# Optimization experiments

Measured on AMD Instinct MI355X. Metric: run time of the kernel, lower is better.

## Reference

```python
import jax, jax.numpy as jnp
import numpy as np

B, H, D = 128, 64, 64  # batch, num_heads, head_dim; einsum structure forces seq n == m == D and H == D


def setup_inputs() -> dict:
    rng = jax.random.key(0)
    ks = jax.random.split(rng, 6)
    query = jax.random.normal(ks[0], (B, H, D, D), jnp.float32)
    key = jax.random.normal(ks[1], (B, H, D, D), jnp.float32) * 0.02
    value = jax.random.normal(ks[2], (B, H, D, D), jnp.float32) * 0.02
    memory_key = jax.random.normal(ks[3], (H, D, D), jnp.float32) * 0.02
    memory_norm = jax.random.uniform(ks[4], (H,), jnp.float32)
    memory_value = jax.random.normal(ks[5], (H, D, D), jnp.float32) * 0.02
    compression_rate = jnp.ones((H,), jnp.float32)
    return {"query": query, "key": key, "value": value,
            "memory_key": memory_key, "memory_norm": memory_norm,
            "memory_value": memory_value, "compression_rate": compression_rate}


def reference(query, key, value, memory_key, memory_norm, memory_value, compression_rate):
    h = memory_norm.shape[0]
    d = memory_key.shape[-1]

    # ---- update(key, value): associative binding + running stats (torch no_grad block) ----
    # binding in fp16 then cast to fp32, exactly as the source einsum does
    binding = jnp.einsum('bhnd,bhmd->bhnm',
                         key.astype(jnp.float16),
                         value.astype(jnp.float16)).astype(jnp.float32)
    mean_binding = binding.reshape(-1, h).mean(axis=0)            # [H] (row-major flatten, as torch .view)
    k_flat = key.reshape(-1, h, d)                                # [B*N, H, D]
    v_flat = value.reshape(-1, h, d)
    mean_value = v_flat.mean(axis=0)                              # [H, D]
    mean_key_norm = jnp.linalg.norm(k_flat.mean(axis=0), axis=-1) # [H]
    # source resets memory_key to zeros [H, D] (shape check always fires), then addcmul_
    new_memory_key = mean_binding[:, None] * mean_value           # [H, D]
    new_memory_norm = memory_norm + mean_key_norm                 # [H]
    # conditional adaptive compression
    factor = jnp.where(new_memory_norm.mean() > 0.9, compression_rate,
                       jnp.ones_like(compression_rate))
    new_memory_key = jax.lax.stop_gradient(new_memory_key * factor[:, None])
    new_memory_norm = jax.lax.stop_gradient(new_memory_norm * factor)

    # ---- retrieve(query): normalized linear-attention readout ----
    scores = jnp.einsum('bhnd,hnm->bhmd',
                        query.astype(jnp.float16),
                        memory_key.astype(jnp.float16)).astype(jnp.float32)
    # source broadcasts memory_norm [H] over the trailing dim (valid since H == D)
    scores = scores / (memory_norm + 1e-6)
    memory_output = jnp.einsum('bhmd,hnm->bhnd', scores, memory_value)
    return memory_output, scores, new_memory_key, new_memory_norm
```

## Files before the change

### kernel.cpp

```cpp
#include <hip/hip_runtime.h>
#include <hip/hip_fp16.h>

typedef _Float16 f16x8 __attribute__((ext_vector_type(8)));
typedef float f32x4 __attribute__((ext_vector_type(4)));

__device__ __forceinline__ f32x4 ntld4(const float* p) {
    return __builtin_nontemporal_load((const f32x4*)p);
}
__device__ __forceinline__ f32x4 ld4(const float* p) {
    return *(const f32x4*)p;
}
__device__ __forceinline__ void ntst4(float* p, f32x4 v) {
    __builtin_nontemporal_store(v, (f32x4*)p);
}

__global__ __launch_bounds__(256) void prep(
    const float* __restrict__ mk, const float* __restrict__ mv,
    _Float16* __restrict__ mkTb, _Float16* __restrict__ Wb)
{
    __shared__ _Float16 mks[64][72];
    __shared__ _Float16 mvs[64][72];
    const int t = threadIdx.x;
    const int h = blockIdx.x;
    const float* mkb = mk + h * 4096;
    const float* mvb = mv + h * 4096;
    {
        const int nn = t >> 2, m0 = (t & 3) * 16;
        f32x4 a0 = ld4(mkb + nn * 64 + m0),     a1 = ld4(mkb + nn * 64 + m0 + 4);
        f32x4 a2 = ld4(mkb + nn * 64 + m0 + 8), a3 = ld4(mkb + nn * 64 + m0 + 12);
        f32x4 b0 = ld4(mvb + nn * 64 + m0),     b1 = ld4(mvb + nn * 64 + m0 + 4);
        f32x4 b2 = ld4(mvb + nn * 64 + m0 + 8), b3 = ld4(mvb + nn * 64 + m0 + 12);
        f16x8 k0, k1, v0, v1;
#pragma unroll
        for (int i = 0; i < 4; ++i) {
            k0[i] = (_Float16)a0[i]; k0[i + 4] = (_Float16)a1[i];
            k1[i] = (_Float16)a2[i]; k1[i + 4] = (_Float16)a3[i];
            v0[i] = (_Float16)b0[i]; v0[i + 4] = (_Float16)b1[i];
            v1[i] = (_Float16)b2[i]; v1[i + 4] = (_Float16)b3[i];
        }
        *(f16x8*)&mks[nn][m0]     = k0;
        *(f16x8*)&mks[nn][m0 + 8] = k1;
        *(f16x8*)&mvs[nn][m0]     = v0;
        *(f16x8*)&mvs[nn][m0 + 8] = v1;
    }
    __syncthreads();
    const int w = t >> 6, l = t & 63, lr = l & 15, lk = l >> 4;
    f32x4 acc[4] = {};
#pragma unroll
    for (int kn = 0; kn < 2; ++kn) {
        f16x8 bfr = *(const f16x8*)&mks[16 * w + lr][kn * 32 + lk * 8];
#pragma unroll
        for (int di = 0; di < 4; ++di) {
            f16x8 afr = *(const f16x8*)&mvs[16 * di + lr][kn * 32 + lk * 8];
            acc[di] = __builtin_amdgcn_mfma_f32_16x16x32_f16(afr, bfr, acc[di], 0, 0, 0);
        }
    }
#pragma unroll
    for (int di = 0; di < 4; ++di)
#pragma unroll
        for (int r = 0; r < 4; ++r)
            Wb[h * 4096 + (16 * di + 4 * lk + r) * 64 + 16 * w + lr] = (_Float16)acc[di][r];
    {
        const int m = t & 63, n0 = (t >> 6) * 16;
        f16x8 x0, x1;
#pragma unroll
        for (int i = 0; i < 8; ++i) { x0[i] = mks[n0 + i][m]; x1[i] = mks[n0 + 8 + i][m]; }
        *(f16x8*)&mkTb[h * 4096 + m * 64 + n0]     = x0;
        *(f16x8*)&mkTb[h * 4096 + m * 64 + n0 + 8] = x1;
    }
}

__global__ __launch_bounds__(256) void mega(
    const float* __restrict__ q,   const float* __restrict__ key,
    const float* __restrict__ val, const _Float16* __restrict__ mkTb,
    const float* __restrict__ mnorm, const _Float16* __restrict__ Wb,
    float* __restrict__ out_mo, float* __restrict__ out_sc,
    float* __restrict__ skp, float* __restrict__ svp, float* __restrict__ pbp,
    const int nbR)
{
    __shared__ struct { float ktile[64][68]; float red[256]; float ks[64]; } smr;

    const int t   = threadIdx.x;
    const int bid = blockIdx.x;

    if (bid < nbR) {
        const int r0 = t >> 4;
        const int c0 = (t & 15) << 2;
        f32x4 ska[4] = {}; f32x4 sva[4] = {};
        float pba[4] = {0.f, 0.f, 0.f, 0.f};
        f32x4 ka[4], va[4];
        int i = bid;
#pragma unroll
        for (int qq = 0; qq < 4; ++qq) {
            const int row = r0 + 16 * qq;
            ka[qq] = ntld4(key + (size_t)i * 4096 + row * 64 + c0);
            va[qq] = ntld4(val + (size_t)i * 4096 + row * 64 + c0);
        }
        while (true) {
            const int inx = i + nbR;
            const bool more = (inx < 8192);
            f32x4 kn4[4], vn4[4];
            if (more) {
#pragma unroll
                for (int qq = 0; qq < 4; ++qq) {
                    const int row = r0 + 16 * qq;
                    kn4[qq] = ntld4(key + (size_t)inx * 4096 + row * 64 + c0);
                    vn4[qq] = ntld4(val + (size_t)inx * 4096 + row * 64 + c0);
                }
            }
#pragma unroll
            for (int qq = 0; qq < 4; ++qq) {
                const int row = r0 + 16 * qq;
                ska[qq] += ka[qq];
                sva[qq] += va[qq];
                *(f32x4*)&smr.ktile[row][c0] = ka[qq];
            }
            __syncthreads();
            {
                const int d  = t & 63;
                const int rr = (t >> 6) * 16;
                float p = 0.f;
#pragma unroll
                for (int r = 0; r < 16; ++r) p += smr.ktile[rr + r][d];
                smr.red[t] = p;
            }
            __syncthreads();
            if (t < 64)
                smr.ks[t] = smr.red[t] + smr.red[t + 64] + smr.red[t + 128] + smr.red[t + 192];
            __syncthreads();
#pragma unroll
            for (int qq = 0; qq < 4; ++qq) {
                float pq = va[qq][0] * smr.ks[c0]     + va[qq][1] * smr.ks[c0 + 1]
                         + va[qq][2] * smr.ks[c0 + 2] + va[qq][3] * smr.ks[c0 + 3];
                pq += __shfl_xor(pq, 1);
                pq += __shfl_xor(pq, 2);
                pq += __shfl_xor(pq, 4);
                pq += __shfl_xor(pq, 8);
                pba[qq] += pq;
            }
            if (!more) break;
#pragma unroll
            for (int qq = 0; qq < 4; ++qq) { ka[qq] = kn4[qq]; va[qq] = vn4[qq]; }
            i = inx;
        }
        const size_t pb4 = (size_t)bid * 4096;
#pragma unroll
        for (int qq = 0; qq < 4; ++qq) {
            ntst4(skp + pb4 + 4 * t + 1024 * qq, ska[qq]);
            ntst4(svp + pb4 + 4 * t + 1024 * qq, sva[qq]);
        }
        if ((t & 15) == 0) {
#pragma unroll
            for (int qq = 0; qq < 4; ++qq)
                pbp[bid * 64 + r0 + 16 * qq] = pba[qq];
        }
        return;
    }

    const int fid = bid - nbR;
    const int h   = fid >> 7;
    const int b   = fid & 127;
    const int bh  = b * 64 + h;
    const float* qb = q + (size_t)bh * 4096;

    const int w  = t >> 6;
    const int l  = t & 63;
    const int lr = l & 15;
    const int lk = l >> 4;

    f16x8 bfrK[2], bfrW[2];
    {
        const _Float16* mrow = mkTb + h * 4096 + (16 * w + lr) * 64 + lk * 8;
        const _Float16* wrow = Wb   + h * 4096 + (16 * w + lr) * 64 + lk * 8;
        bfrK[0] = *(const f16x8*)(mrow);
        bfrK[1] = *(const f16x8*)(mrow + 32);
        bfrW[0] = *(const f16x8*)(wrow);
        bfrW[1] = *(const f16x8*)(wrow + 32);
    }
    f32x4 scl[4];
#pragma unroll
    for (int di = 0; di < 4; ++di) {
        f32x4 nv = ld4(mnorm + 16 * di + 4 * lk);
#pragma unroll
        for (int r = 0; r < 4; ++r) scl[di][r] = __builtin_amdgcn_rcpf(nv[r] + 1e-6f);
    }

    f16x8 afr[4][2];
#pragma unroll
    for (int di = 0; di < 4; ++di) {
        const float* qcol = qb + 16 * di + lr;
#pragma unroll
        for (int kn = 0; kn < 2; ++kn) {
            const float* p0 = qcol + (kn * 32 + lk * 8) * 64;
            f16x8 a;
#pragma unroll
            for (int e = 0; e < 8; ++e) a[e] = (_Float16)p0[e * 64];
            afr[di][kn] = a;
        }
    }

    f32x4 accS[4] = {}, accO[4] = {};
#pragma unroll
    for (int kn = 0; kn < 2; ++kn) {
#pragma unroll
        for (int di = 0; di < 4; ++di) {
            accS[di] = __builtin_amdgcn_mfma_f32_16x16x32_f16(afr[di][kn], bfrK[kn], accS[di], 0, 0, 0);
            accO[di] = __builtin_amdgcn_mfma_f32_16x16x32_f16(afr[di][kn], bfrW[kn], accO[di], 0, 0, 0);
        }
    }

    const int m = 16 * w + lr;
    const size_t gbase = (size_t)bh * 4096;
#pragma unroll
    for (int di = 0; di < 4; ++di) {
        const int d0 = 16 * di + 4 * lk;
        f32x4 sv, ov;
#pragma unroll
        for (int r = 0; r < 4; ++r) {
            sv[r] = accS[di][r] * scl[di][r];
            ov[r] = accO[di][r] * scl[di][r];
        }
        ntst4(out_sc + gbase + (size_t)m * 64 + d0, sv);
        ntst4(out_mo + gbase + (size_t)m * 64 + d0, ov);
    }
}

#define NCHUNK 8
__global__ __launch_bounds__(256) void reduce2(
    const float* __restrict__ skp, const float* __restrict__ svp,
    const float* __restrict__ pbp, float* __restrict__ p2,
    const int nbR, const int clen)
{
    const int bi = blockIdx.x;
    const int c  = bi / 33;
    const int e  = (bi % 33) * 256 + threadIdx.x;
    if (e >= 8256) return;
    int n0 = c * clen;
    int n1 = n0 + clen; if (n1 > nbR) n1 = nbR;
    float s = 0.f;
    if (e < 4096) {
        for (int n = n0; n < n1; ++n) s += skp[(size_t)n * 4096 + e];
    } else if (e < 8192) {
        const int e2 = e - 4096;
        for (int n = n0; n < n1; ++n) s += svp[(size_t)n * 4096 + e2];
    } else {
        const int e2 = e - 8192;
        for (int n = n0; n < n1; ++n) s += pbp[n * 64 + e2];
    }
    p2[c * 8256 + e] = s;
}

__global__ __launch_bounds__(256) void finalize(
    const float* __restrict__ p2, const float* __restrict__ mnorm,
    const float* __restrict__ crate,
    float* __restrict__ out_nmk, float* __restrict__ out_nmn)
{
    __shared__ float tot[8256];
    __shared__ float fac_s[64];
    const int t = threadIdx.x;
    for (int e = t; e < 8256; e += 256) {
        float s = 0.f;
#pragma unroll
        for (int c = 0; c < NCHUNK; ++c) s += p2[c * 8256 + e];
        tot[e] = s;
    }
    __syncthreads();
    const float* sk_tot = tot;
    const float* sv_tot = tot + 4096;
    const float* pb_tot = tot + 8192;
    if (t < 64) {
        float ss = 0.f;
#pragma unroll 8
        for (int dd = 0; dd < 64; ++dd) {
            float mkm = sk_tot[t * 64 + dd] * (1.0f / 8192.0f);
            ss += mkm * mkm;
        }
        const float nmn = mnorm[t] + sqrtf(ss);
        float v = nmn;
        for (int off = 32; off; off >>= 1) v += __shfl_xor(v, off);
        const float mean = v * (1.0f / 64.0f);
        const float f = (mean > 0.9f) ? crate[t] : 1.0f;
        fac_s[t] = f;
        out_nmn[t] = nmn * f;
    }
    __syncthreads();
    for (int e = t; e < 4096; e += 256) {
        const int jh = e >> 6;
        const float mb = pb_tot[jh] * (1.0f / 524288.0f);
        const float mvv = sv_tot[e] * (1.0f / 8192.0f);
        out_nmk[e] = mb * mvv * fac_s[jh];
    }
}

extern "C" void kernel_launch(void* const* d_in, const int* in_sizes, int n_in,
                              void* d_out, int out_size, void* d_ws, size_t ws_size,
                              hipStream_t stream) {
    const float* q  = (const float*)d_in[0];
    const float* k  = (const float*)d_in[1];
    const float* v  = (const float*)d_in[2];
    const float* mk = (const float*)d_in[3];
    const float* mn = (const float*)d_in[4];
    const float* mv = (const float*)d_in[5];
    const float* cr = (const float*)d_in[6];

    float* out     = (float*)d_out;
    float* out_mo  = out;
    float* out_sc  = out + 33554432;
    float* out_nmk = out + 67108864;
    float* out_nmn = out + 67112960;

    float* ws   = (float*)d_ws;
    float* p2   = ws;
    _Float16* mkTb = (_Float16*)(ws + NCHUNK * 8256);
    _Float16* Wb   = mkTb + 64 * 4096;
    float* part = ws + NCHUNK * 8256 + 262144;
    const size_t wsf = ws_size / 4;
    const size_t used = NCHUNK * 8256 + 262144;
    const size_t avail = (wsf > used) ? (wsf - used) : 0;
    int nb = (int)(avail / 8256);
    if (nb > 256) nb = 256;
    if (nb < 1)   nb = 1;
    float* skp = part;
    float* svp = part + (size_t)nb * 4096;
    float* pbp = svp  + (size_t)nb * 4096;
    const int clen = (nb + NCHUNK - 1) / NCHUNK;

    hipLaunchKernelGGL(prep, dim3(64), dim3(256), 0, stream,
                       mk, mv, mkTb, Wb);
    hipLaunchKernelGGL(mega, dim3(nb + 8192), dim3(256), 0, stream,
                       q, k, v, mkTb, mn, Wb, out_mo, out_sc, skp, svp, pbp, nb);
    hipLaunchKernelGGL(reduce2, dim3(33 * NCHUNK), dim3(256), 0, stream,
                       skp, svp, pbp, p2, nb, clen);
    hipLaunchKernelGGL(finalize, dim3(1), dim3(256), 0, stream,
                       p2, mn, cr, out_nmk, out_nmn);
}
```

Measured before the change: 157.7 us.

## Assign one (b,h) tile per wavefront instead of per block in retrieve path

Each wavefront now computes a full 64x64 output tile for its own (b,h) pair, so the retrieve grid shrinks by four. Before, each block split one tile across four waves, and every wave loaded the same 64x64 query block into registers. That redundant fp32 query load is gone, and query loads now use nontemporal hints. In exchange each wave issues four times more MFMAs and holds larger accumulator arrays, which raises register pressure and may lower occupancy.

```diff
diff --git a/kernel.cpp b/kernel.cpp
--- a/kernel.cpp
+++ b/kernel.cpp
@@ -6,6 +6,9 @@
 
 __device__ __forceinline__ f32x4 ntld4(const float* p) {
     return __builtin_nontemporal_load((const f32x4*)p);
+}
+__device__ __forceinline__ float ntld1(const float* p) {
+    return __builtin_nontemporal_load(p);
 }
 __device__ __forceinline__ f32x4 ld4(const float* p) {
     return *(const f32x4*)p;
@@ -157,34 +160,16 @@
         return;
     }
 
-    const int fid = bid - nbR;
+    const int fid = (bid - nbR) * 4 + (t >> 6);
     const int h   = fid >> 7;
     const int b   = fid & 127;
     const int bh  = b * 64 + h;
     const float* qb = q + (size_t)bh * 4096;
 
-    const int w  = t >> 6;
     const int l  = t & 63;
     const int lr = l & 15;
     const int lk = l >> 4;
 
-    f16x8 bfrK[2], bfrW[2];
-    {
-        const _Float16* mrow = mkTb + h * 4096 + (16 * w + lr) * 64 + lk * 8;
-        const _Float16* wrow = Wb   + h * 4096 + (16 * w + lr) * 64 + lk * 8;
-        bfrK[0] = *(const f16x8*)(mrow);
-        bfrK[1] = *(const f16x8*)(mrow + 32);
-        bfrW[0] = *(const f16x8*)(wrow);
-        bfrW[1] = *(const f16x8*)(wrow + 32);
-    }
-    f32x4 scl[4];
-#pragma unroll
-    for (int di = 0; di < 4; ++di) {
-        f32x4 nv = ld4(mnorm + 16 * di + 4 * lk);
-#pragma unroll
-        for (int r = 0; r < 4; ++r) scl[di][r] = __builtin_amdgcn_rcpf(nv[r] + 1e-6f);
-    }
-
     f16x8 afr[4][2];
 #pragma unroll
     for (int di = 0; di < 4; ++di) {
@@ -194,34 +179,73 @@
             const float* p0 = qcol + (kn * 32 + lk * 8) * 64;
             f16x8 a;
 #pragma unroll
-            for (int e = 0; e < 8; ++e) a[e] = (_Float16)p0[e * 64];
+            for (int e = 0; e < 8; ++e) a[e] = (_Float16)ntld1(p0 + e * 64);
             afr[di][kn] = a;
         }
     }
 
-    f32x4 accS[4] = {}, accO[4] = {};
-#pragma unroll
-    for (int kn = 0; kn < 2; ++kn) {
-#pragma unroll
-        for (int di = 0; di < 4; ++di) {
-            accS[di] = __builtin_amdgcn_mfma_f32_16x16x32_f16(afr[di][kn], bfrK[kn], accS[di], 0, 0, 0);
-            accO[di] = __builtin_amdgcn_mfma_f32_16x16x32_f16(afr[di][kn], bfrW[kn], accO[di], 0, 0, 0);
-        }
-    }
-
-    const int m = 16 * w + lr;
+    f32x4 scl[4];
+#pragma unroll
+    for (int di = 0; di < 4; ++di) {
+        f32x4 nv = ld4(mnorm + 16 * di + 4 * lk);
+#pragma unroll
+        for (int r = 0; r < 4; ++r) scl[di][r] = __builtin_amdgcn_rcpf(nv[r] + 1e-6f);
+    }
+
     const size_t gbase = (size_t)bh * 4096;
-#pragma unroll
-    for (int di = 0; di < 4; ++di) {
-        const int d0 = 16 * di + 4 * lk;
-        f32x4 sv, ov;
-#pragma unroll
-        for (int r = 0; r < 4; ++r) {
-            sv[r] = accS[di][r] * scl[di][r];
-            ov[r] = accO[di][r] * scl[di][r];
-        }
-        ntst4(out_sc + gbase + (size_t)m * 64 + d0, sv);
-        ntst4(out_mo + gbase + (size_t)m * 64 + d0, ov);
+
+    {
+        f32x4 accS[4][4] = {};
+#pragma unroll
+        for (int ms = 0; ms < 4; ++ms) {
+            const _Float16* mrow = mkTb + h * 4096 + (16 * ms + lr) * 64 + lk * 8;
+            f16x8 bk0 = *(const f16x8*)(mrow);
+            f16x8 bk1 = *(const f16x8*)(mrow + 32);
+#pragma unroll
+            for (int di = 0; di < 4; ++di) {
+                accS[ms][di] = __builtin_amdgcn_mfma_f32_16x16x32_f16(afr[di][0], bk0, accS[ms][di], 0, 0, 0);
+                accS[ms][di] = __builtin_amdgcn_mfma_f32_16x16x32_f16(afr[di][1], bk1, accS[ms][di], 0, 0, 0);
+            }
+        }
+#pragma unroll
+        for (int ms = 0; ms < 4; ++ms) {
+            const int m = 16 * ms + lr;
+#pragma unroll
+            for (int di = 0; di < 4; ++di) {
+                const int d0 = 16 * di + 4 * lk;
+                f32x4 sv;
+#pragma unroll
+                for (int r = 0; r < 4; ++r) sv[r] = accS[ms][di][r] * scl[di][r];
+                ntst4(out_sc + gbase + (size_t)m * 64 + d0, sv);
+            }
+        }
+    }
+
+    {
+        f32x4 accO[4][4] = {};
+#pragma unroll
+        for (int ms = 0; ms < 4; ++ms) {
+            const _Float16* wrow = Wb + h * 4096 + (16 * ms + lr) * 64 + lk * 8;
+            f16x8 bw0 = *(const f16x8*)(wrow);
+            f16x8 bw1 = *(const f16x8*)(wrow + 32);
+#pragma unroll
+            for (int di = 0; di < 4; ++di) {
+                accO[ms][di] = __builtin_amdgcn_mfma_f32_16x16x32_f16(afr[di][0], bw0, accO[ms][di], 0, 0, 0);
+                accO[ms][di] = __builtin_amdgcn_mfma_f32_16x16x32_f16(afr[di][1], bw1, accO[ms][di], 0, 0, 0);
+            }
+        }
+#pragma unroll
+        for (int ms = 0; ms < 4; ++ms) {
+            const int m = 16 * ms + lr;
+#pragma unroll
+            for (int di = 0; di < 4; ++di) {
+                const int d0 = 16 * di + 4 * lk;
+                f32x4 ov;
+#pragma unroll
+                for (int r = 0; r < 4; ++r) ov[r] = accO[ms][di][r] * scl[di][r];
+                ntst4(out_mo + gbase + (size_t)m * 64 + d0, ov);
+            }
+        }
     }
 }
 
@@ -327,7 +351,7 @@
 
     hipLaunchKernelGGL(prep, dim3(64), dim3(256), 0, stream,
                        mk, mv, mkTb, Wb);
-    hipLaunchKernelGGL(mega, dim3(nb + 8192), dim3(256), 0, stream,
+    hipLaunchKernelGGL(mega, dim3(nb + 2048), dim3(256), 0, stream,
                        q, k, v, mkTb, mn, Wb, out_mo, out_sc, skp, svp, pbp, nb);
     hipLaunchKernelGGL(reduce2, dim3(33 * NCHUNK), dim3(256), 0, stream,
                        skp, svp, pbp, p2, nb, clen);
```

Result: slower. 188.7 us (+19.7%).
